# Performance work log

Hardware: AMD Instinct MI355X
Metric: run time of the kernel (lower is better)

## Reference

```python
import jax, jax.numpy as jnp
import numpy as np

C = 96        # channels
NH = 4        # num_heads
WIN = (2, 2, 2)
B, D, H, W = 2, 48, 48, 48
HID = 4 * C   # FFN hidden dim
EPS = 1e-5


def setup_inputs() -> dict:
    key = jax.random.key(0)
    ks = iter(jax.random.split(key, 64))
    def nrm(shape, scale=0.02):
        return jax.random.normal(next(ks), shape, jnp.float32) * scale
    inp = {
        "fg_feature": jax.random.normal(next(ks), (B, C, D, H, W), jnp.float32),
        "bg_feature": jax.random.normal(next(ks), (B, C, D, H, W), jnp.float32),
    }
    for p in ("fg", "bg"):
        inp[f"{p}_qn_w"] = jnp.ones((C,), jnp.float32)
        inp[f"{p}_qn_b"] = jnp.zeros((C,), jnp.float32)
        inp[f"{p}_kvn_w"] = jnp.ones((C,), jnp.float32)
        inp[f"{p}_kvn_b"] = jnp.zeros((C,), jnp.float32)
        inp[f"{p}_attn_in_w"] = nrm((3 * C, C))
        inp[f"{p}_attn_in_b"] = jnp.zeros((3 * C,), jnp.float32)
        inp[f"{p}_attn_out_w"] = nrm((C, C))
        inp[f"{p}_attn_out_b"] = jnp.zeros((C,), jnp.float32)
        inp[f"{p}_ffn_n_w"] = jnp.ones((C,), jnp.float32)
        inp[f"{p}_ffn_n_b"] = jnp.zeros((C,), jnp.float32)
        inp[f"{p}_ffn_w1"] = nrm((HID, C))
        inp[f"{p}_ffn_b1"] = jnp.zeros((HID,), jnp.float32)
        inp[f"{p}_ffn_w2"] = nrm((C, HID))
        inp[f"{p}_ffn_b2"] = jnp.zeros((C,), jnp.float32)
        inp[f"{p}_conv_w"] = nrm((C, C))  # 1x1x1 Conv3d kernel flattened to [Cout,Cin]
        inp[f"{p}_conv_b"] = jnp.zeros((C,), jnp.float32)
        inp[f"{p}_in_w"] = jnp.ones((C,), jnp.float32)
        inp[f"{p}_in_b"] = jnp.zeros((C,), jnp.float32)
    return inp


def _gelu(x):
    return jax.nn.gelu(x, approximate=False)  # torch nn.GELU default (erf)


def _ln(x, w, b):
    m = x.mean(-1, keepdims=True)
    v = ((x - m) ** 2).mean(-1, keepdims=True)
    return (x - m) * jax.lax.rsqrt(v + EPS) * w + b


def _window_partition(x):
    b, c, d, h, w = x.shape
    wd, wh, ww = WIN
    x = x.reshape(b, c, d // wd, wd, h // wh, wh, w // ww, ww)
    x = x.transpose(0, 2, 4, 6, 3, 5, 7, 1)
    return x.reshape(-1, wd * wh * ww, c)  # [num_windows, 8, C]


def _window_reverse(t, shape):
    b, c, d, h, w = shape
    wd, wh, ww = WIN
    x = t.reshape(b, d // wd, h // wh, w // ww, wd, wh, ww, c)
    x = x.transpose(0, 7, 1, 4, 2, 5, 3, 6)
    return x.reshape(b, c, d, h, w)


def _mha(q, k, v, Wi, bi, Wo, bo):
    # torch MultiheadAttention with packed in_proj, batch_first
    N, Lq, c = q.shape
    dh = c // NH
    qp = (q @ Wi[:c].T + bi[:c]).reshape(N, Lq, NH, dh)
    kp = (k @ Wi[c:2 * c].T + bi[c:2 * c]).reshape(N, -1, NH, dh)
    vp = (v @ Wi[2 * c:].T + bi[2 * c:]).reshape(N, -1, NH, dh)
    att = jnp.einsum('nqhd,nkhd->nhqk', qp, kp) * (1.0 / np.sqrt(dh))
    att = jax.nn.softmax(att, axis=-1)
    o = jnp.einsum('nhqk,nkhd->nqhd', att, vp).reshape(N, Lq, c)
    return o @ Wo.T + bo


def _ffn(x, w1, b1, w2, b2):
    return _gelu(x @ w1.T + b1) @ w2.T + b2


def _proj(x, cw, cb, iw, ib):
    # 1x1x1 Conv3d -> InstanceNorm3d(affine) -> GELU
    y = jnp.einsum('bcdhw,oc->bodhw', x, cw) + cb[None, :, None, None, None]
    m = y.mean((2, 3, 4), keepdims=True)
    v = ((y - m) ** 2).mean((2, 3, 4), keepdims=True)
    y = (y - m) * jax.lax.rsqrt(v + EPS)
    y = y * iw[None, :, None, None, None] + ib[None, :, None, None, None]
    return _gelu(y)


def _forward(fg_feature, bg_feature,
             fg_qn_w, fg_qn_b, fg_kvn_w, fg_kvn_b,
             fg_attn_in_w, fg_attn_in_b, fg_attn_out_w, fg_attn_out_b,
             fg_ffn_n_w, fg_ffn_n_b, fg_ffn_w1, fg_ffn_b1, fg_ffn_w2, fg_ffn_b2,
             fg_conv_w, fg_conv_b, fg_in_w, fg_in_b,
             bg_qn_w, bg_qn_b, bg_kvn_w, bg_kvn_b,
             bg_attn_in_w, bg_attn_in_b, bg_attn_out_w, bg_attn_out_b,
             bg_ffn_n_w, bg_ffn_n_b, bg_ffn_w1, bg_ffn_b1, bg_ffn_w2, bg_ffn_b2,
             bg_conv_w, bg_conv_b, bg_in_w, bg_in_b):
    meta = fg_feature.shape
    fg_t = _window_partition(fg_feature)
    bg_t = _window_partition(bg_feature)
    fg_q = _ln(fg_t, fg_qn_w, fg_qn_b)
    bg_q = _ln(bg_t, bg_qn_w, bg_qn_b)
    fg_c = _ln(fg_t, fg_kvn_w, fg_kvn_b)
    bg_c = _ln(bg_t, bg_kvn_w, bg_kvn_b)
    fg_t = fg_t + _mha(fg_q, bg_c, bg_c, fg_attn_in_w, fg_attn_in_b, fg_attn_out_w, fg_attn_out_b)
    bg_t = bg_t + _mha(bg_q, fg_c, fg_c, bg_attn_in_w, bg_attn_in_b, bg_attn_out_w, bg_attn_out_b)
    fg_t = fg_t + _ffn(_ln(fg_t, fg_ffn_n_w, fg_ffn_n_b), fg_ffn_w1, fg_ffn_b1, fg_ffn_w2, fg_ffn_b2)
    bg_t = bg_t + _ffn(_ln(bg_t, bg_ffn_n_w, bg_ffn_n_b), bg_ffn_w1, bg_ffn_b1, bg_ffn_w2, bg_ffn_b2)
    fg = _window_reverse(fg_t, meta)
    bg = _window_reverse(bg_t, meta)
    fg = _proj(fg, fg_conv_w, fg_conv_b, fg_in_w, fg_in_b)
    bg = _proj(bg, bg_conv_w, bg_conv_b, bg_in_w, bg_in_b)
    return fg, bg


def reference(fg_feature, bg_feature,
              fg_qn_w, fg_qn_b, fg_kvn_w, fg_kvn_b,
              fg_attn_in_w, fg_attn_in_b, fg_attn_out_w, fg_attn_out_b,
              fg_ffn_n_w, fg_ffn_n_b, fg_ffn_w1, fg_ffn_b1, fg_ffn_w2, fg_ffn_b2,
              fg_conv_w, fg_conv_b, fg_in_w, fg_in_b,
              bg_qn_w, bg_qn_b, bg_kvn_w, bg_kvn_b,
              bg_attn_in_w, bg_attn_in_b, bg_attn_out_w, bg_attn_out_b,
              bg_ffn_n_w, bg_ffn_n_b, bg_ffn_w1, bg_ffn_b1, bg_ffn_w2, bg_ffn_b2,
              bg_conv_w, bg_conv_b, bg_in_w, bg_in_b):
    return _forward(fg_feature, bg_feature,
                    fg_qn_w, fg_qn_b, fg_kvn_w, fg_kvn_b,
                    fg_attn_in_w, fg_attn_in_b, fg_attn_out_w, fg_attn_out_b,
                    fg_ffn_n_w, fg_ffn_n_b, fg_ffn_w1, fg_ffn_b1, fg_ffn_w2, fg_ffn_b2,
                    fg_conv_w, fg_conv_b, fg_in_w, fg_in_b,
                    bg_qn_w, bg_qn_b, bg_kvn_w, bg_kvn_b,
                    bg_attn_in_w, bg_attn_in_b, bg_attn_out_w, bg_attn_out_b,
                    bg_ffn_n_w, bg_ffn_n_b, bg_ffn_w1, bg_ffn_b1, bg_ffn_w2, bg_ffn_b2,
                    bg_conv_w, bg_conv_b, bg_in_w, bg_in_b)
```

## Files before the change

### kernel.cpp

```cpp
#include <hip/hip_runtime.h>
#include <hip/hip_bf16.h>


#define G_TOK 221184
#define TOK_PER_B 110592
#define STREAM_ELEMS 21233664

typedef __attribute__((ext_vector_type(8))) short short8;
typedef __attribute__((ext_vector_type(4))) float f32x4;
typedef unsigned short ushort_t;
typedef unsigned int uint_t;

#define MFMA16 __builtin_amdgcn_mfma_f32_16x16x32_bf16

__device__ __forceinline__ float gelu_erf(float x) {
    return 0.5f * x * (1.0f + erff(x * 0.70710678118654752f));
}
__device__ __forceinline__ float gelu_tanh(float x) {
    float u = x * (1.5957691216f + 0.0713548163f * x * x);
    return x / (1.0f + __expf(-u));
}
__device__ __forceinline__ ushort_t bfb(float f) {
    __hip_bfloat16 h = __float2bfloat16(f);
    return *reinterpret_cast<ushort_t*>(&h);
}
__device__ __forceinline__ void unpack8(uint4 v, float* o) {
    o[0] = __uint_as_float(v.x << 16); o[1] = __uint_as_float(v.x & 0xffff0000u);
    o[2] = __uint_as_float(v.y << 16); o[3] = __uint_as_float(v.y & 0xffff0000u);
    o[4] = __uint_as_float(v.z << 16); o[5] = __uint_as_float(v.z & 0xffff0000u);
    o[6] = __uint_as_float(v.w << 16); o[7] = __uint_as_float(v.w & 0xffff0000u);
}
__device__ __forceinline__ uint4 pack8(const float* f) {
    uint4 v;
    v.x = (uint_t)bfb(f[0]) | ((uint_t)bfb(f[1]) << 16);
    v.y = (uint_t)bfb(f[2]) | ((uint_t)bfb(f[3]) << 16);
    v.z = (uint_t)bfb(f[4]) | ((uint_t)bfb(f[5]) << 16);
    v.w = (uint_t)bfb(f[6]) | ((uint_t)bfb(f[7]) << 16);
    return v;
}
__device__ __forceinline__ uint2 pack4(const float* f) {
    uint2 v;
    v.x = (uint_t)bfb(f[0]) | ((uint_t)bfb(f[1]) << 16);
    v.y = (uint_t)bfb(f[2]) | ((uint_t)bfb(f[3]) << 16);
    return v;
}
__device__ __forceinline__ short8 pks8(const float* f) {
    short8 r;
    #pragma unroll
    for (int j = 0; j < 8; ++j) r[j] = (short)bfb(f[j]);
    return r;
}

__global__ __launch_bounds__(256) void k_fold(
    const float* __restrict__ Wi, const float* __restrict__ bi,
    const float* __restrict__ Wo, const float* __restrict__ bo,
    const float* __restrict__ W1, const float* __restrict__ b1,
    const float* __restrict__ W2, const float* __restrict__ b2,
    const float* __restrict__ Wc,
    const float* __restrict__ qnw, const float* __restrict__ qnb,
    const float* __restrict__ kvw, const float* __restrict__ kvb,
    const float* __restrict__ fnw, const float* __restrict__ fnb,
    ushort_t* __restrict__ w, float* __restrict__ bs)
{
    const float scale = 0.20412414523193150f;
    int tid0 = blockIdx.x * 256 + threadIdx.x;
    int nth = gridDim.x * 256;
    for (int o = tid0; o < 120672; o += nth) {
        if (o < 36864) {
            int blkid = o / 9216, oo = o % 9216;
            int e = oo & 7, fid = (oo >> 3) & 63, g = oo >> 9;
            int t = g / 3, u = g % 3, l15 = fid >> 2, kb = fid & 3;
            int c = t * 16 + l15, k = u * 32 + kb * 8 + e;
            float v;
            if (blkid == 0)      v = Wi[c * 96 + k] * qnw[k] * scale;
            else if (blkid == 1) v = Wi[(96 + c) * 96 + k] * kvw[k];
            else if (blkid == 2) v = Wi[(192 + c) * 96 + k] * kvw[k];
            else                 v = Wo[c * 96 + k];
            w[o] = bfb(v);
        } else if (o < 110592) {
            int oo = o - 36864; int half = oo / 36864; oo %= 36864;
            int e = oo & 7, fid = (oo >> 3) & 63, g = oo >> 9;
            int ch = g / 18, r = g % 18, tt = r / 3, u = r % 3;
            int l15 = fid >> 2, kb = fid & 3;
            float v;
            if (half == 0) {
                int c = ch * 96 + tt * 16 + l15, k = u * 32 + kb * 8 + e;
                v = W1[c * 96 + k] * fnw[k];
            } else {
                int c = tt * 16 + l15, k = ch * 96 + u * 32 + kb * 8 + e;
                v = W2[c * 384 + k];
            }
            w[o] = bfb(v);
        } else if (o < 119808) {
            int oo = o - 110592;
            int e = oo & 7, fid = (oo >> 3) & 63, g = oo >> 9;
            int t = g / 3, u = g % 3, l15 = fid >> 2, kb = fid & 3;
            w[o] = bfb(Wc[(t * 16 + l15) * 96 + u * 32 + kb * 8 + e]);
        } else {
            int x = o - 119808;
            if (x < 96) {
                float s = bi[x];
                #pragma unroll 4
                for (int k = 0; k < 96; ++k) s += qnb[k] * Wi[x * 96 + k];
                bs[x] = s * scale;
            } else if (x < 192) {
                int c = x - 96; float s = bi[96 + c];
                #pragma unroll 4
                for (int k = 0; k < 96; ++k) s += kvb[k] * Wi[(96 + c) * 96 + k];
                bs[x] = s;
            } else if (x < 288) {
                int c = x - 192; float s = bi[192 + c];
                #pragma unroll 4
                for (int k = 0; k < 96; ++k) s += kvb[k] * Wi[(192 + c) * 96 + k];
                bs[x] = s;
            } else if (x < 384) {
                bs[x] = bo[x - 288];
            } else if (x < 768) {
                int c = x - 384; float s = b1[c];
                #pragma unroll 4
                for (int k = 0; k < 96; ++k) s += fnb[k] * W1[c * 96 + k];
                bs[x] = s;
            } else {
                bs[x] = b2[x - 768];
            }
        }
    }
}

__global__ __launch_bounds__(256) void k_gather(
    const float* __restrict__ srcf, const float* __restrict__ srcb,
    ushort_t* __restrict__ Xf, ushort_t* __restrict__ Xb)
{
    __shared__ float tile[192 * 97];
    int blk = blockIdx.x;
    const float* src; ushort_t* X;
    if (blk < 1152) { src = srcf; X = Xf; }
    else            { src = srcb; X = Xb; blk -= 1152; }
    int b = blk / 576, rem = blk % 576, dw = rem / 24, hw = rem % 24;
    int tid = threadIdx.x;
    for (int i = tid; i < 384 * 48; i += 256) {
        int r = i / 48, w = i % 48;
        int c = r >> 2, d_off = (r >> 1) & 1, h_off = r & 1;
        float v = src[((((long)b * 96 + c) * 48 + dw * 2 + d_off) * 48 + hw * 2 + h_off) * 48 + w];
        int t = (w >> 1) * 8 + d_off * 4 + h_off * 2 + (w & 1);
        tile[t * 97 + c] = v;
    }
    __syncthreads();
    long base = ((((long)b * 24 + dw) * 24 + hw) * 24) * 8;
    for (int i = tid; i < 192 * 12; i += 256) {
        int t = i / 12, c8 = i % 12;
        *(uint4*)&X[(base + t) * 96 + c8 * 8] = pack8(&tile[t * 97 + c8 * 8]);
    }
}

__device__ __forceinline__ void gemmT_stage(
    const short8* xb2, const ushort_t* __restrict__ W,
    const float* __restrict__ bias, ushort_t* outs,
    int mbase, int l15, int kb, int fid)
{
    #pragma unroll
    for (int t = 0; t < 6; ++t) {
        float4 bv = *(const float4*)&bias[t * 16 + kb * 4];
        f32x4 A0 = {bv.x, bv.y, bv.z, bv.w};
        f32x4 A1 = {bv.x, bv.y, bv.z, bv.w};
        #pragma unroll
        for (int u = 0; u < 3; ++u) {
            short8 bw = *(const short8*)&W[(t * 3 + u) * 512 + fid * 8];
            A0 = MFMA16(bw, xb2[u],     A0, 0, 0, 0);
            A1 = MFMA16(bw, xb2[3 + u], A1, 0, 0, 0);
        }
        float f0[4], f1[4];
        #pragma unroll
        for (int i = 0; i < 4; ++i) { f0[i] = A0[i]; f1[i] = A1[i]; }
        *(uint2*)&outs[(mbase + l15) * 104 + t * 16 + kb * 4]      = pack4(f0);
        *(uint2*)&outs[(mbase + 16 + l15) * 104 + t * 16 + kb * 4] = pack4(f1);
    }
}

__global__ __launch_bounds__(256, 2) void k_attn(
    ushort_t* __restrict__ Xf, ushort_t* __restrict__ Xb,
    const ushort_t* __restrict__ wf, const ushort_t* __restrict__ wb,
    const float* __restrict__ bsf, const float* __restrict__ bsb)
{
    __shared__ ushort_t qs[128 * 104];
    __shared__ ushort_t kv[128 * 104];
    int tid = threadIdx.x, lane = tid & 63, wv = tid >> 6, mbase = wv * 32;
    int l15 = lane & 15, kb = lane >> 4, fid = l15 * 4 + kb;
    long g0 = (long)blockIdx.x * 128;

    short8 fr[2][6];
    #pragma unroll
    for (int s = 0; s < 2; ++s) {
        #pragma unroll
        for (int m = 0; m < 2; ++m) {
            const ushort_t* px = (s ? Xb : Xf) + (g0 + mbase + m * 16 + l15) * 96 + kb * 8;
            float f[24];
            unpack8(*(const uint4*)px, f);
            unpack8(*(const uint4*)(px + 32), f + 8);
            unpack8(*(const uint4*)(px + 64), f + 16);
            float s1 = 0.f, s2 = 0.f;
            #pragma unroll
            for (int j = 0; j < 24; ++j) { s1 += f[j]; s2 += f[j] * f[j]; }
            s1 += __shfl_xor(s1, 16); s1 += __shfl_xor(s1, 32);
            s2 += __shfl_xor(s2, 16); s2 += __shfl_xor(s2, 32);
            float mm = s1 * (1.f / 96.f);
            float rr = rsqrtf(s2 * (1.f / 96.f) - mm * mm + 1e-5f);
            #pragma unroll
            for (int j = 0; j < 24; ++j) f[j] = (f[j] - mm) * rr;
            fr[s][m * 3 + 0] = pks8(f);
            fr[s][m * 3 + 1] = pks8(f + 8);
            fr[s][m * 3 + 2] = pks8(f + 16);
        }
    }

    #pragma unroll
    for (int dir = 0; dir < 2; ++dir) {
        const ushort_t* W = dir ? wb : wf;
        const float* bs = dir ? bsb : bsf;
        ushort_t* X = dir ? Xb : Xf;

        gemmT_stage(fr[dir],     W,        bs,      qs, mbase, l15, kb, fid);
        gemmT_stage(fr[dir ^ 1], W + 9216, bs + 96, kv, mbase, l15, kb, fid);

        float sc[2][8], inv[2];
        #pragma unroll
        for (int it = 0; it < 2; ++it) {
            int idx = lane + 64 * it;
            int win = (idx >> 5) & 3, hd = (idx >> 3) & 3, q8 = idx & 7;
            int tq = mbase + win * 8 + q8, ko = hd * 24;
            float qf[24];
            #pragma unroll
            for (int u = 0; u < 3; ++u)
                unpack8(*(const uint4*)&qs[tq * 104 + ko + u * 8], qf + u * 8);
            float mx = -1e30f;
            #pragma unroll
            for (int j = 0; j < 8; ++j) {
                float s = 0.f;
                #pragma unroll
                for (int u = 0; u < 3; ++u) {
                    float kf[8];
                    unpack8(*(const uint4*)&kv[(mbase + win * 8 + j) * 104 + ko + u * 8], kf);
                    #pragma unroll
                    for (int d = 0; d < 8; ++d) s += qf[u * 8 + d] * kf[d];
                }
                sc[it][j] = s; mx = fmaxf(mx, s);
            }
            float sum = 0.f;
            #pragma unroll
            for (int j = 0; j < 8; ++j) { sc[it][j] = __expf(sc[it][j] - mx); sum += sc[it][j]; }
            inv[it] = 1.f / sum;
        }

        gemmT_stage(fr[dir ^ 1], W + 18432, bs + 192, kv, mbase, l15, kb, fid);

        #pragma unroll
        for (int it = 0; it < 2; ++it) {
            int idx = lane + 64 * it;
            int win = (idx >> 5) & 3, hd = (idx >> 3) & 3, q8 = idx & 7;
            int tq = mbase + win * 8 + q8, ko = hd * 24;
            #pragma unroll
            for (int u = 0; u < 3; ++u) {
                float of8[8];
                #pragma unroll
                for (int d = 0; d < 8; ++d) of8[d] = 0.f;
                #pragma unroll
                for (int j = 0; j < 8; ++j) {
                    float vf[8];
                    unpack8(*(const uint4*)&kv[(mbase + win * 8 + j) * 104 + ko + u * 8], vf);
                    #pragma unroll
                    for (int d = 0; d < 8; ++d) of8[d] += sc[it][j] * vf[d];
                }
                #pragma unroll
                for (int d = 0; d < 8; ++d) of8[d] *= inv[it];
                *(uint4*)&qs[tq * 104 + ko + u * 8] = pack8(of8);
            }
        }

        {
            short8 o0[6];
            #pragma unroll
            for (int m = 0; m < 2; ++m)
                #pragma unroll
                for (int u = 0; u < 3; ++u)
                    o0[m * 3 + u] = *(const short8*)&qs[(mbase + m * 16 + l15) * 104 + u * 32 + kb * 8];
            gemmT_stage(o0, W + 27648, bs + 288, qs, mbase, l15, kb, fid);
        }
        #pragma unroll
        for (int u = 0; u < 6; ++u) {
            int idx = lane + 64 * u;
            int r2 = idx / 12, c8 = idx % 12;
            ushort_t* p = X + (g0 + mbase + r2) * 96 + c8 * 8;
            float xv[8], av[8], o[8];
            unpack8(*(const uint4*)p, xv);
            unpack8(*(const uint4*)&qs[(mbase + r2) * 104 + c8 * 8], av);
            #pragma unroll
            for (int j = 0; j < 8; ++j) o[j] = xv[j] + av[j];
            *(uint4*)p = pack8(o);
        }
    }
}

__global__ __launch_bounds__(256, 2) void k_ffn(
    ushort_t* __restrict__ Xf, ushort_t* __restrict__ Xb,
    const ushort_t* __restrict__ wf, const ushort_t* __restrict__ wb,
    const float* __restrict__ bsf, const float* __restrict__ bsb)
{
    __shared__ ushort_t H[128 * 104];
    __shared__ ushort_t WB[18432];
    int blk = blockIdx.x, tid = threadIdx.x;
    ushort_t* X; const ushort_t* W; const float* bs;
    if (blk < 1728) { X = Xf; W = wf; bs = bsf; }
    else            { X = Xb; W = wb; bs = bsb; blk -= 1728; }
    long g0 = (long)blk * 128;
    int lane = tid & 63, wv = tid >> 6, mbase = wv * 32;
    int l15 = lane & 15, kb = lane >> 4, fid = l15 * 4 + kb;

    short8 xb2[6];
    #pragma unroll
    for (int m = 0; m < 2; ++m) {
        const ushort_t* px = X + (g0 + mbase + m * 16 + l15) * 96 + kb * 8;
        float f[24];
        unpack8(*(const uint4*)px, f);
        unpack8(*(const uint4*)(px + 32), f + 8);
        unpack8(*(const uint4*)(px + 64), f + 16);
        float s1 = 0.f, s2 = 0.f;
        #pragma unroll
        for (int j = 0; j < 24; ++j) { s1 += f[j]; s2 += f[j] * f[j]; }
        s1 += __shfl_xor(s1, 16); s1 += __shfl_xor(s1, 32);
        s2 += __shfl_xor(s2, 16); s2 += __shfl_xor(s2, 32);
        float mm = s1 * (1.f / 96.f);
        float rr = rsqrtf(s2 * (1.f / 96.f) - mm * mm + 1e-5f);
        #pragma unroll
        for (int j = 0; j < 24; ++j) f[j] = (f[j] - mm) * rr;
        xb2[m * 3 + 0] = pks8(f); xb2[m * 3 + 1] = pks8(f + 8); xb2[m * 3 + 2] = pks8(f + 16);
    }

    const ushort_t* W1 = W + 36864;
    const ushort_t* W2 = W + 73728;
    const ushort_t* Wc = W + 110592;
    const float* b1 = bs + 384;
    const float* b2 = bs + 768;

    f32x4 acc2[2][6];
    #pragma unroll
    for (int t = 0; t < 6; ++t) {
        float4 bv = *(const float4*)&b2[t * 16 + kb * 4];
        acc2[0][t] = {bv.x, bv.y, bv.z, bv.w};
        acc2[1][t] = {bv.x, bv.y, bv.z, bv.w};
    }
    for (int ch = 0; ch < 4; ++ch) {
        {
            const uint4* s1 = (const uint4*)(W1 + ch * 9216);
            const uint4* s2 = (const uint4*)(W2 + ch * 9216);
            uint4* d = (uint4*)WB;
            #pragma unroll
            for (int i = 0; i < 5; ++i) {
                int idx = tid + i * 256;
                if (idx < 1152) { d[idx] = s1[idx]; d[1152 + idx] = s2[idx]; }
            }
        }
        __syncthreads();
        #pragma unroll
        for (int t = 0; t < 6; ++t) {
            float4 bv = *(const float4*)&b1[ch * 96 + t * 16 + kb * 4];
            f32x4 A0 = {bv.x, bv.y, bv.z, bv.w};
            f32x4 A1 = {bv.x, bv.y, bv.z, bv.w};
            #pragma unroll
            for (int u = 0; u < 3; ++u) {
                short8 bw = *(const short8*)&WB[(t * 3 + u) * 512 + fid * 8];
                A0 = MFMA16(bw, xb2[u],     A0, 0, 0, 0);
                A1 = MFMA16(bw, xb2[3 + u], A1, 0, 0, 0);
            }
            float q0[4], q1[4];
            #pragma unroll
            for (int i = 0; i < 4; ++i) { q0[i] = gelu_tanh(A0[i]); q1[i] = gelu_tanh(A1[i]); }
            *(uint2*)&H[(mbase + l15) * 104 + t * 16 + kb * 4]      = pack4(q0);
            *(uint2*)&H[(mbase + 16 + l15) * 104 + t * 16 + kb * 4] = pack4(q1);
        }
        short8 h0[3], h1[3];
        #pragma unroll
        for (int u = 0; u < 3; ++u) {
            h0[u] = *(const short8*)&H[(mbase + l15) * 104 + u * 32 + kb * 8];
            h1[u] = *(const short8*)&H[(mbase + 16 + l15) * 104 + u * 32 + kb * 8];
        }
        #pragma unroll
        for (int t = 0; t < 6; ++t) {
            #pragma unroll
            for (int u = 0; u < 3; ++u) {
                short8 bw = *(const short8*)&WB[9216 + (t * 3 + u) * 512 + fid * 8];
                acc2[0][t] = MFMA16(bw, h0[u], acc2[0][t], 0, 0, 0);
                acc2[1][t] = MFMA16(bw, h1[u], acc2[1][t], 0, 0, 0);
            }
        }
        __syncthreads();
    }
    {
        const uint4* sc_ = (const uint4*)Wc;
        uint4* d = (uint4*)WB;
        #pragma unroll
        for (int i = 0; i < 5; ++i) {
            int idx = tid + i * 256;
            if (idx < 1152) d[idx] = sc_[idx];
        }
    }
    #pragma unroll
    for (int t = 0; t < 6; ++t) {
        float f0[4], f1[4];
        #pragma unroll
        for (int i = 0; i < 4; ++i) { f0[i] = acc2[0][t][i]; f1[i] = acc2[1][t][i]; }
        *(uint2*)&H[(mbase + l15) * 104 + t * 16 + kb * 4]      = pack4(f0);
        *(uint2*)&H[(mbase + 16 + l15) * 104 + t * 16 + kb * 4] = pack4(f1);
    }
    #pragma unroll
    for (int u = 0; u < 6; ++u) {
        int idx = lane + 64 * u;
        int r2 = idx / 12, c8 = idx % 12;
        float xv[8], fv[8], y[8];
        unpack8(*(const uint4*)(X + (g0 + mbase + r2) * 96 + c8 * 8), xv);
        unpack8(*(const uint4*)&H[(mbase + r2) * 104 + c8 * 8], fv);
        #pragma unroll
        for (int j = 0; j < 8; ++j) y[j] = xv[j] + fv[j];
        *(uint4*)&H[(mbase + r2) * 104 + c8 * 8] = pack8(y);
    }
    __syncthreads();
    short8 y0[3], y1[3];
    #pragma unroll
    for (int u = 0; u < 3; ++u) {
        y0[u] = *(const short8*)&H[(mbase + l15) * 104 + u * 32 + kb * 8];
        y1[u] = *(const short8*)&H[(mbase + 16 + l15) * 104 + u * 32 + kb * 8];
    }
    #pragma unroll
    for (int t = 0; t < 6; ++t) {
        f32x4 A0 = {0.f, 0.f, 0.f, 0.f}, A1 = {0.f, 0.f, 0.f, 0.f};
        #pragma unroll
        for (int u = 0; u < 3; ++u) {
            short8 bw = *(const short8*)&WB[(t * 3 + u) * 512 + fid * 8];
            A0 = MFMA16(bw, y0[u], A0, 0, 0, 0);
            A1 = MFMA16(bw, y1[u], A1, 0, 0, 0);
        }
        float o0[4], o1[4];
        #pragma unroll
        for (int i = 0; i < 4; ++i) { o0[i] = A0[i]; o1[i] = A1[i]; }
        *(uint2*)&H[(mbase + l15) * 104 + t * 16 + kb * 4]      = pack4(o0);
        *(uint2*)&H[(mbase + 16 + l15) * 104 + t * 16 + kb * 4] = pack4(o1);
    }
    #pragma unroll
    for (int u = 0; u < 6; ++u) {
        int idx = lane + 64 * u;
        int r2 = idx / 12, c8 = idx % 12;
        *(uint4*)(X + (g0 + mbase + r2) * 96 + c8 * 8) =
            *(const uint4*)&H[(mbase + r2) * 104 + c8 * 8];
    }
}

__global__ __launch_bounds__(384) void k_instats(
    const ushort_t* __restrict__ Xf, const ushort_t* __restrict__ Xb,
    float* __restrict__ partial)
{
    __shared__ float red[2][32][96];
    int blk = blockIdx.x;
    const ushort_t* X = (blk < 108) ? Xf : Xb;
    int rem = blk % 108;
    int b = rem / 54, chunk = rem % 54;
    int tid = threadIdx.x;
    int c8 = tid % 12, slot = tid / 12;
    long base = (long)b * TOK_PER_B + chunk * 2048;
    float s8[8], ss8[8];
    #pragma unroll
    for (int j = 0; j < 8; ++j) { s8[j] = 0.f; ss8[j] = 0.f; }
    for (int i = 0; i < 64; ++i) {
        long row = base + i * 32 + slot;
        float f[8];
        unpack8(*(const uint4*)&X[row * 96 + c8 * 8], f);
        #pragma unroll
        for (int j = 0; j < 8; ++j) { s8[j] += f[j]; ss8[j] += f[j] * f[j]; }
    }
    #pragma unroll
    for (int j = 0; j < 8; ++j) {
        red[0][slot][c8 * 8 + j] = s8[j];
        red[1][slot][c8 * 8 + j] = ss8[j];
    }
    __syncthreads();
    if (tid < 96) {
        float S = 0.f, SS = 0.f;
        for (int sl = 0; sl < 32; ++sl) { S += red[0][sl][tid]; SS += red[1][sl][tid]; }
        partial[((long)blockIdx.x * 96 + tid) * 2]     = S;
        partial[((long)blockIdx.x * 96 + tid) * 2 + 1] = SS;
    }
}

__global__ __launch_bounds__(384) void k_infin(
    const float* __restrict__ partial, float* __restrict__ inMR)
{
    int tid = threadIdx.x;
    int s = tid / 192, rem = tid % 192, b = rem / 96, c = rem % 96;
    float S = 0.f, SS = 0.f;
    for (int ch = 0; ch < 54; ++ch) {
        int blk = s * 108 + b * 54 + ch;
        S  += partial[(blk * 96 + c) * 2];
        SS += partial[(blk * 96 + c) * 2 + 1];
    }
    float m = S * (1.f / 110592.f);
    float var = SS * (1.f / 110592.f) - m * m;
    inMR[tid * 2] = m;
    inMR[tid * 2 + 1] = rsqrtf(var + 1e-5f);
}

__global__ __launch_bounds__(256) void k_scatter(
    const ushort_t* __restrict__ Xf, const ushort_t* __restrict__ Xb,
    const float* __restrict__ inMR,
    const float* __restrict__ iwf, const float* __restrict__ ibf,
    const float* __restrict__ iwb, const float* __restrict__ ibb,
    float* __restrict__ out)
{
    __shared__ float tile[192 * 97];
    int blk = blockIdx.x, s = 0;
    const ushort_t* X = Xf; const float* iw = iwf; const float* ib = ibf;
    if (blk >= 1152) { s = 1; X = Xb; iw = iwb; ib = ibb; blk -= 1152; }
    int b = blk / 576, rem = blk % 576, dw = rem / 24, hw = rem % 24;
    int tid = threadIdx.x;
    long base = ((((long)b * 24 + dw) * 24 + hw) * 24) * 8;
    for (int i = tid; i < 192 * 12; i += 256) {
        int t = i / 12, c8 = i % 12;
        float f[8]; unpack8(*(const uint4*)&X[(base + t) * 96 + c8 * 8], f);
        #pragma unroll
        for (int j = 0; j < 8; ++j) tile[t * 97 + c8 * 8 + j] = f[j];
    }
    __syncthreads();
    float* o = out + (long)s * STREAM_ELEMS;
    for (int i = tid; i < 384 * 48; i += 256) {
        int r = i / 48, w = i % 48;
        int c = r >> 2, d_off = (r >> 1) & 1, h_off = r & 1;
        int t = (w >> 1) * 8 + d_off * 4 + h_off * 2 + (w & 1);
        float v = tile[t * 97 + c];
        float m  = inMR[((s * 2 + b) * 96 + c) * 2];
        float rr = inMR[((s * 2 + b) * 96 + c) * 2 + 1];
        v = (v - m) * rr * iw[c] + ib[c];
        o[((((long)b * 96 + c) * 48 + dw * 2 + d_off) * 48 + hw * 2 + h_off) * 48 + w] = gelu_erf(v);
    }
}

extern "C" void kernel_launch(void* const* d_in, const int* in_sizes, int n_in,
                              void* d_out, int out_size, void* d_ws, size_t ws_size,
                              hipStream_t stream)
{
    #define IN(i) ((const float*)d_in[i])
    ushort_t* Xf = (ushort_t*)d_ws;
    ushort_t* Xb = Xf + (long)STREAM_ELEMS;
    ushort_t* wW  = Xb + (long)STREAM_ELEMS;
    ushort_t* wWb = wW + 119808;
    float* bsf = (float*)(wWb + 119808);
    float* bsb = bsf + 864;
    float* partial = bsb + 864;
    float* inMR = partial + 41472;

    k_fold<<<128, 256, 0, stream>>>(IN(6), IN(7), IN(8), IN(9), IN(12), IN(13), IN(14), IN(15), IN(16),
                                    IN(2), IN(3), IN(22), IN(23), IN(10), IN(11), wW, bsf);
    k_fold<<<128, 256, 0, stream>>>(IN(24), IN(25), IN(26), IN(27), IN(30), IN(31), IN(32), IN(33), IN(34),
                                    IN(20), IN(21), IN(4), IN(5), IN(28), IN(29), wWb, bsb);

    k_gather<<<2304, 256, 0, stream>>>(IN(0), IN(1), Xf, Xb);

    k_attn<<<1728, 256, 0, stream>>>(Xf, Xb, wW, wWb, bsf, bsb);

    k_ffn<<<3456, 256, 0, stream>>>(Xf, Xb, wW, wWb, bsf, bsb);

    k_instats<<<216, 384, 0, stream>>>(Xf, Xb, partial);
    k_infin<<<1, 384, 0, stream>>>(partial, inMR);

    k_scatter<<<2304, 256, 0, stream>>>(Xf, Xb, inMR,
                                        IN(18), IN(19), IN(36), IN(37),
                                        (float*)d_out);
    #undef IN
}
```

Before: 616.3 us.

## Stage attention weights in LDS and use lane-contiguous weight fragment layout

The packed-weight layout now puts each fragment at lane*8 (l15 + 16*kb) instead of (l15*4+kb)*8, so a wavefront's 16-byte weight loads are contiguous and bank-friendly. The attention kernel now copies each 96x96 projection block into a new 18 KB shared buffer before its MFMA stage, where it previously read weights straight from global memory. This adds several block barriers per direction and raises LDS use per block, which may cut occupancy under launch_bounds(256,2). The dir loop is also no longer unrolled.

```diff
diff --git a/kernel.cpp b/kernel.cpp
--- a/kernel.cpp
+++ b/kernel.cpp
@@ -68,8 +68,8 @@
     for (int o = tid0; o < 120672; o += nth) {
         if (o < 36864) {
             int blkid = o / 9216, oo = o % 9216;
-            int e = oo & 7, fid = (oo >> 3) & 63, g = oo >> 9;
-            int t = g / 3, u = g % 3, l15 = fid >> 2, kb = fid & 3;
+            int e = oo & 7, ln = (oo >> 3) & 63, g = oo >> 9;
+            int t = g / 3, u = g % 3, l15 = ln & 15, kb = ln >> 4;
             int c = t * 16 + l15, k = u * 32 + kb * 8 + e;
             float v;
             if (blkid == 0)      v = Wi[c * 96 + k] * qnw[k] * scale;
@@ -79,9 +79,9 @@
             w[o] = bfb(v);
         } else if (o < 110592) {
             int oo = o - 36864; int half = oo / 36864; oo %= 36864;
-            int e = oo & 7, fid = (oo >> 3) & 63, g = oo >> 9;
+            int e = oo & 7, ln = (oo >> 3) & 63, g = oo >> 9;
             int ch = g / 18, r = g % 18, tt = r / 3, u = r % 3;
-            int l15 = fid >> 2, kb = fid & 3;
+            int l15 = ln & 15, kb = ln >> 4;
             float v;
             if (half == 0) {
                 int c = ch * 96 + tt * 16 + l15, k = u * 32 + kb * 8 + e;
@@ -93,8 +93,8 @@
             w[o] = bfb(v);
         } else if (o < 119808) {
             int oo = o - 110592;
-            int e = oo & 7, fid = (oo >> 3) & 63, g = oo >> 9;
-            int t = g / 3, u = g % 3, l15 = fid >> 2, kb = fid & 3;
+            int e = oo & 7, ln = (oo >> 3) & 63, g = oo >> 9;
+            int t = g / 3, u = g % 3, l15 = ln & 15, kb = ln >> 4;
             w[o] = bfb(Wc[(t * 16 + l15) * 96 + u * 32 + kb * 8 + e]);
         } else {
             int x = o - 119808;
@@ -153,11 +153,22 @@
     }
 }
 
+__device__ __forceinline__ void stageW(ushort_t* WB, const ushort_t* Wsrc, int tid) {
+    const uint4* s = (const uint4*)Wsrc;
+    uint4* d = (uint4*)WB;
+    #pragma unroll
+    for (int i = 0; i < 5; ++i) {
+        int idx = tid + i * 256;
+        if (idx < 1152) d[idx] = s[idx];
+    }
+}
+
 __device__ __forceinline__ void gemmT_stage(
     const short8* xb2, const ushort_t* __restrict__ W,
     const float* __restrict__ bias, ushort_t* outs,
-    int mbase, int l15, int kb, int fid)
-{
+    int mbase, int l15, int kb)
+{
+    const int ln8 = (kb * 16 + l15) * 8;
     #pragma unroll
     for (int t = 0; t < 6; ++t) {
         float4 bv = *(const float4*)&bias[t * 16 + kb * 4];
@@ -165,7 +176,7 @@
         f32x4 A1 = {bv.x, bv.y, bv.z, bv.w};
         #pragma unroll
         for (int u = 0; u < 3; ++u) {
-            short8 bw = *(const short8*)&W[(t * 3 + u) * 512 + fid * 8];
+            short8 bw = *(const short8*)&W[(t * 3 + u) * 512 + ln8];
             A0 = MFMA16(bw, xb2[u],     A0, 0, 0, 0);
             A1 = MFMA16(bw, xb2[3 + u], A1, 0, 0, 0);
         }
@@ -184,8 +195,9 @@
 {
     __shared__ ushort_t qs[128 * 104];
     __shared__ ushort_t kv[128 * 104];
+    __shared__ ushort_t WB[9216];
     int tid = threadIdx.x, lane = tid & 63, wv = tid >> 6, mbase = wv * 32;
-    int l15 = lane & 15, kb = lane >> 4, fid = l15 * 4 + kb;
+    int l15 = lane & 15, kb = lane >> 4;
     long g0 = (long)blockIdx.x * 128;
 
     short8 fr[2][6];
@@ -213,14 +225,16 @@
         }
     }
 
-    #pragma unroll
     for (int dir = 0; dir < 2; ++dir) {
         const ushort_t* W = dir ? wb : wf;
         const float* bs = dir ? bsb : bsf;
         ushort_t* X = dir ? Xb : Xf;
 
-        gemmT_stage(fr[dir],     W,        bs,      qs, mbase, l15, kb, fid);
-        gemmT_stage(fr[dir ^ 1], W + 9216, bs + 96, kv, mbase, l15, kb, fid);
+        stageW(WB, W, tid);            __syncthreads();
+        gemmT_stage(fr[dir], WB, bs, qs, mbase, l15, kb);
+        __syncthreads();
+        stageW(WB, W + 9216, tid);     __syncthreads();
+        gemmT_stage(fr[dir ^ 1], WB, bs + 96, kv, mbase, l15, kb);
 
         float sc[2][8], inv[2];
         #pragma unroll
@@ -250,8 +264,9 @@
             for (int j = 0; j < 8; ++j) { sc[it][j] = __expf(sc[it][j] - mx); sum += sc[it][j]; }
             inv[it] = 1.f / sum;
         }
-
-        gemmT_stage(fr[dir ^ 1], W + 18432, bs + 192, kv, mbase, l15, kb, fid);
+        __syncthreads();
+        stageW(WB, W + 18432, tid);    __syncthreads();
+        gemmT_stage(fr[dir ^ 1], WB, bs + 192, kv, mbase, l15, kb);
 
         #pragma unroll
         for (int it = 0; it < 2; ++it) {
@@ -275,7 +290,8 @@
                 *(uint4*)&qs[tq * 104 + ko + u * 8] = pack8(of8);
             }
         }
-
+        __syncthreads();
+        stageW(WB, W + 27648, tid);    __syncthreads();
         {
             short8 o0[6];
             #pragma unroll
@@ -283,7 +299,7 @@
                 #pragma unroll
                 for (int u = 0; u < 3; ++u)
                     o0[m * 3 + u] = *(const short8*)&qs[(mbase + m * 16 + l15) * 104 + u * 32 + kb * 8];
-            gemmT_stage(o0, W + 27648, bs + 288, qs, mbase, l15, kb, fid);
+            gemmT_stage(o0, WB, bs + 288, qs, mbase, l15, kb);
         }
         #pragma unroll
         for (int u = 0; u < 6; ++u) {
@@ -297,6 +313,7 @@
             for (int j = 0; j < 8; ++j) o[j] = xv[j] + av[j];
             *(uint4*)p = pack8(o);
         }
+        __syncthreads();
     }
 }
 
@@ -313,7 +330,8 @@
     else            { X = Xb; W = wb; bs = bsb; blk -= 1728; }
     long g0 = (long)blk * 128;
     int lane = tid & 63, wv = tid >> 6, mbase = wv * 32;
-    int l15 = lane & 15, kb = lane >> 4, fid = l15 * 4 + kb;
+    int l15 = lane & 15, kb = lane >> 4;
+    const int ln8 = lane * 8;
 
     short8 xb2[6];
     #pragma unroll
@@ -367,7 +385,7 @@
             f32x4 A1 = {bv.x, bv.y, bv.z, bv.w};
             #pragma unroll
             for (int u = 0; u < 3; ++u) {
-                short8 bw = *(const short8*)&WB[(t * 3 + u) * 512 + fid * 8];
+                short8 bw = *(const short8*)&WB[(t * 3 + u) * 512 + ln8];
                 A0 = MFMA16(bw, xb2[u],     A0, 0, 0, 0);
                 A1 = MFMA16(bw, xb2[3 + u], A1, 0, 0, 0);
             }
@@ -387,7 +405,7 @@
         for (int t = 0; t < 6; ++t) {
             #pragma unroll
             for (int u = 0; u < 3; ++u) {
-                short8 bw = *(const short8*)&WB[9216 + (t * 3 + u) * 512 + fid * 8];
+                short8 bw = *(const short8*)&WB[9216 + (t * 3 + u) * 512 + ln8];
                 acc2[0][t] = MFMA16(bw, h0[u], acc2[0][t], 0, 0, 0);
                 acc2[1][t] = MFMA16(bw, h1[u], acc2[1][t], 0, 0, 0);
             }
@@ -434,7 +452,7 @@
         f32x4 A0 = {0.f, 0.f, 0.f, 0.f}, A1 = {0.f, 0.f, 0.f, 0.f};
         #pragma unroll
         for (int u = 0; u < 3; ++u) {
-            short8 bw = *(const short8*)&WB[(t * 3 + u) * 512 + fid * 8];
+            short8 bw = *(const short8*)&WB[(t * 3 + u) * 512 + ln8];
             A0 = MFMA16(bw, y0[u], A0, 0, 0, 0);
             A1 = MFMA16(bw, y1[u], A1, 0, 0, 0);
         }
```

New measurement: 637.0 us. +3.4%, slower.
